# Kernel optimization log

Hardware: AMD Instinct MI355X
Metric: run time of the kernel (lower is better)

## Reference

```python
import jax, jax.numpy as jnp
import numpy as np

Q = 4096  # num_quantizing
E = 256   # quantizing_dim


def setup_inputs() -> dict:
    key = jax.random.key(0)
    kx, kw = jax.random.split(key)
    x = jax.random.normal(kx, (16, 2048, E), dtype=jnp.float32)
    # nn.init.normal_(weight, mean=0.0, std=0.001)
    weight = 0.001 * jax.random.normal(kw, (Q, E), dtype=jnp.float32)
    return {"x": x, "weight": weight}


def reference(x, weight):
    # x: (*, E), weight: (Q, E)
    input_shape = x.shape
    xf = x.reshape(-1, weight.shape[1])  # (N, E)
    # Squared L2 distance via norm expansion (same argmin as sum(delta^2)):
    x2 = jnp.sum(xf * xf, axis=1, keepdims=True)          # (N, 1)
    w2 = jnp.sum(weight * weight, axis=1)                  # (Q,)
    dist = x2 - 2.0 * (xf @ weight.T) + w2                 # (N, Q)
    q_idx = jnp.argmin(dist, axis=1)                       # (N,)
    q_data = weight[q_idx]                                 # (N, E)
    return q_data.reshape(input_shape), q_idx.reshape(input_shape[:-1])
```

## Files before the change

### kernel.cpp

```cpp
#include <hip/hip_runtime.h>
#include <cfloat>
#include <climits>

constexpr int E  = 256;
constexpr int Qn = 4096;
constexpr float WSCALE = 4096.0f;


typedef _Float16 half8  __attribute__((ext_vector_type(8)));
typedef _Float16 half4v __attribute__((ext_vector_type(4)));
typedef float    f32x16 __attribute__((ext_vector_type(16)));

#define GAS __attribute__((address_space(1)))
#define LAS __attribute__((address_space(3)))

#define NEG_INF __int_as_float(0xFF800000)

__device__ inline bool lexlt(float a, int ai, float b, int bi) {
    return a < b || (a == b && ai < bi);
}

__global__ __launch_bounds__(256) void prep_kernel(
    const float* __restrict__ x, const float* __restrict__ w,
    _Float16* __restrict__ A16, _Float16* __restrict__ B16,
    float* __restrict__ w2, int nxblocks)
{
    int blk  = blockIdx.x;
    int sub  = threadIdx.x >> 6;
    int lane = threadIdx.x & 63;
    bool isX = blk < nxblocks;
    int row  = (isX ? blk : blk - nxblocks) * 4 + sub;

    const float* src = isX ? x : w;
    float4 v = *(const float4*)(src + (size_t)row * E + lane * 4);

    if (!isX) {
        float s = v.x * v.x + v.y * v.y + v.z * v.z + v.w * v.w;
        #pragma unroll
        for (int off = 32; off; off >>= 1) s += __shfl_xor(s, off);
        if (lane == 0) w2[row] = s;
    }

    float sc = isX ? 1.0f : WSCALE;
    half4v h = { (_Float16)(v.x * sc), (_Float16)(v.y * sc),
                 (_Float16)(v.z * sc), (_Float16)(v.w * sc) };
    _Float16* dst16 = (isX ? A16 : B16) + (size_t)row * 256;
    *(half4v*)(dst16 + lane * 4) = h;
}

__device__ inline void ins4max(float K[4], float k) {
    #pragma unroll
    for (int t = 0; t < 4; ++t) {
        float mx = fmaxf(K[t], k);
        k = fminf(K[t], k);
        K[t] = mx;
    }
}

union SmemU {
    _Float16 buf[4][2][128][64];
    float2 mergeS[128 * 16];
};

#define KSTEP(T, VMSTR, Q, H)                                              \
  {                                                                        \
    asm volatile("s_waitcnt " VMSTR ::: "memory");                         \
    __builtin_amdgcn_s_barrier();                                          \
    asm volatile("" ::: "memory");                                         \
    const int t_ = (T);                                                    \
    if (t_ + 3 < 64) stage_t(t_ + 3);                                      \
    const _Float16* Wb = &sm.buf[t_ & 3][0][0][0];                         \
    if ((H) == 0) { acc0 = (f32x16){}; acc1 = (f32x16){}; }                \
    __builtin_amdgcn_s_setprio(1);                                         \
    _Pragma("unroll")                                                      \
    for (int ktl = 0; ktl < 2; ++ktl)                                      \
      _Pragma("unroll")                                                    \
      for (int s = 0; s < 4; ++s) {                                        \
        int kc = 2 * s + lh;                                               \
        half8 wf = *(const half8*)(Wb + ktl * 8192                         \
                      + fr * 64 + ((kc ^ frsw) << 3));                     \
        acc0 = __builtin_amdgcn_mfma_f32_32x32x16_f16(                     \
                   wf, xf[0][2 * (H) + ktl][s], acc0, 0, 0, 0);            \
        acc1 = __builtin_amdgcn_mfma_f32_32x32x16_f16(                     \
                   wf, xf[1][2 * (H) + ktl][s], acc1, 0, 0, 0);            \
      }                                                                    \
    __builtin_amdgcn_s_setprio(0);                                         \
    if ((H) == 1) {                                                        \
      const int ct_ = t_ >> 1;                                             \
      _Pragma("unroll")                                                    \
      for (int r = 0; r < 16; ++r) {                                       \
        int crow = (r & 3) + 8 * (r >> 2) + 4 * lh;                        \
        int qg   = ct_ * 128 + cwg * 32 + crow;                            \
        float pk0 = __int_as_float(                                        \
            (__float_as_int(acc0[r]) & 0xFFFFF000) | qg);                  \
        t2[0][(Q)] = __builtin_amdgcn_fmed3f(t1[0][(Q)], t2[0][(Q)], pk0); \
        t1[0][(Q)] = fmaxf(t1[0][(Q)], pk0);                               \
        float pk1 = __int_as_float(                                        \
            (__float_as_int(acc1[r]) & 0xFFFFF000) | qg);                  \
        t2[1][(Q)] = __builtin_amdgcn_fmed3f(t1[1][(Q)], t2[1][(Q)], pk1); \
        t1[1][(Q)] = fmaxf(t1[1][(Q)], pk1);                               \
      }                                                                    \
    }                                                                      \
  }

__global__ __launch_bounds__(512, 2) void vq_mfma_kernel(
    const _Float16* __restrict__ A16,
    const _Float16* __restrict__ B16,
    float4* __restrict__ top4)
{
    __shared__ SmemU sm;

    const int tid  = threadIdx.x;
    const int wv   = tid >> 6;
    const int lane = tid & 63;
    const int l31  = lane & 31;
    const int lh   = lane >> 5;
    const int rb   = blockIdx.x;

    const int cwg = wv & 3;
    const int rg  = wv >> 2;

    const int srow = lane >> 3;
    const int schk = lane & 7;

    const _Float16* Ab16 = A16 + (size_t)rb * 128 * 256;

    auto stage_half = [&](const _Float16* src, int slot, int h) {
        #pragma unroll
        for (int ktl = 0; ktl < 2; ++ktl)
            #pragma unroll
            for (int i = 0; i < 2; ++i) {
                int row  = i * 64 + wv * 8 + srow;
                int gchk = schk ^ (row & 7);
                const _Float16* g = src + (size_t)row * 256
                                    + (2 * h + ktl) * 64 + gchk * 8;
                __builtin_amdgcn_global_load_lds((const GAS void*)g,
                    (LAS void*)(&sm.buf[slot][ktl][i * 64 + wv * 8][0]),
                    16, 0, 0);
            }
    };
    auto stage_t = [&](int t) {
        stage_half(B16 + (size_t)(t >> 1) * 128 * 256, t & 3, t & 1);
    };

    stage_half(Ab16, 0, 0);
    stage_half(Ab16, 1, 1);
    __syncthreads();

    half8 xf[2][4][4];
    #pragma unroll
    for (int n = 0; n < 2; ++n)
        #pragma unroll
        for (int kt = 0; kt < 4; ++kt)
            #pragma unroll
            for (int s = 0; s < 4; ++s) {
                int xr = rg * 64 + n * 32 + l31;
                int kc = 2 * s + lh;
                xf[n][kt][s] = *(const half8*)(&sm.buf[kt >> 1][kt & 1][0][0]
                                + xr * 64 + ((kc ^ (xr & 7)) << 3));
            }
    __syncthreads();

    stage_t(0); stage_t(1); stage_t(2);

    float t1[2][4], t2[2][4];
    #pragma unroll
    for (int n = 0; n < 2; ++n)
        #pragma unroll
        for (int q = 0; q < 4; ++q) { t1[n][q] = NEG_INF; t2[n][q] = NEG_INF; }

    const int fr   = cwg * 32 + l31;
    const int frsw = fr & 7;

    f32x16 acc0, acc1;

    #pragma unroll
    for (int q = 0; q < 4; ++q) {
        const int nct = (q == 3) ? 7 : 8;
        for (int ctt = 0; ctt < nct; ++ctt) {
            const int t0 = (q * 8 + ctt) * 2;
            KSTEP(t0,     "vmcnt(8)", q, 0);
            KSTEP(t0 + 1, "vmcnt(8)", q, 1);
        }
    }
    KSTEP(62, "vmcnt(4)", 3, 0);
    KSTEP(63, "vmcnt(0)", 3, 1);

    #pragma unroll
    for (int n = 0; n < 2; ++n)
        #pragma unroll
        for (int q = 0; q < 4; ++q) {
            float o1 = __shfl_xor(t1[n][q], 32);
            float o2 = __shfl_xor(t2[n][q], 32);
            float m1 = fmaxf(t1[n][q], o1);
            float m2 = __builtin_amdgcn_fmed3f(t1[n][q], o1,
                                               fmaxf(t2[n][q], o2));
            t1[n][q] = m1; t2[n][q] = m2;
        }

    __syncthreads();

    if (lh == 0) {
        #pragma unroll
        for (int n = 0; n < 2; ++n) {
            int row = rg * 64 + n * 32 + l31;
            #pragma unroll
            for (int q = 0; q < 4; ++q)
                sm.mergeS[row * 16 + cwg * 4 + q] =
                    make_float2(t1[n][q], t2[n][q]);
        }
    }
    __syncthreads();

    if (tid < 128) {
        float K[4] = { NEG_INF, NEG_INF, NEG_INF, NEG_INF };
        #pragma unroll
        for (int sl = 0; sl < 16; ++sl) {
            float2 a = sm.mergeS[tid * 16 + sl];
            ins4max(K, a.x);
            ins4max(K, a.y);
        }
        top4[(size_t)rb * 128 + tid] = make_float4(K[0], K[1], K[2], K[3]);
    }
}

__global__ __launch_bounds__(256) void finalize_kernel(
    const float4* __restrict__ top4, const float* __restrict__ x,
    const float* __restrict__ w, const float* __restrict__ w2,
    float* __restrict__ qdata, float* __restrict__ qidx)
{
    int row  = blockIdx.x * 4 + (threadIdx.x >> 6);
    int lane = threadIdx.x & 63;

    float4 c4 = top4[row];
    int chosen[4] = { __float_as_int(c4.x) & 0xFFF,
                      __float_as_int(c4.y) & 0xFFF,
                      __float_as_int(c4.z) & 0xFFF,
                      __float_as_int(c4.w) & 0xFFF };

    float4 xv = *(const float4*)(x + (size_t)row * E + lane * 4);
    float s2 = xv.x * xv.x + xv.y * xv.y + xv.z * xv.z + xv.w * xv.w;
    float d[4];
    #pragma unroll
    for (int j = 0; j < 4; ++j) {
        float4 wv = *(const float4*)(w + (size_t)chosen[j] * E + lane * 4);
        d[j] = xv.x * wv.x + xv.y * wv.y + xv.z * wv.z + xv.w * wv.w;
    }
    #pragma unroll
    for (int off = 32; off; off >>= 1) {
        s2 += __shfl_xor(s2, off);
        #pragma unroll
        for (int j = 0; j < 4; ++j) d[j] += __shfl_xor(d[j], off);
    }

    float bs = FLT_MAX; int win = INT_MAX;
    #pragma unroll
    for (int j = 0; j < 4; ++j) {
        float s = (s2 - 2.0f * d[j]) + w2[chosen[j]];
        if (lexlt(s, chosen[j], bs, win)) { bs = s; win = chosen[j]; }
    }

    if (lane == 0) qidx[row] = (float)win;
    *(float4*)(qdata + (size_t)row * E + lane * 4) =
        *(const float4*)(w + (size_t)win * E + lane * 4);
}

constexpr int FBM = 64, FBN = 128, FBK = 64, FPAD = 4, FTH = 256;

__global__ __launch_bounds__(64) void row_sumsq_kernel(const float* __restrict__ src,
                                                       float* __restrict__ dst) {
    int row = blockIdx.x, lane = threadIdx.x;
    float4 v = ((const float4*)(src + (size_t)row * E))[lane];
    float s = v.x * v.x + v.y * v.y + v.z * v.z + v.w * v.w;
    #pragma unroll
    for (int off = 32; off > 0; off >>= 1) s += __shfl_down(s, off);
    if (lane == 0) dst[row] = s;
}

__global__ __launch_bounds__(FTH) void vq_fallback_kernel(
    const float* __restrict__ x, const float* __restrict__ w,
    const float* __restrict__ x2, const float* __restrict__ w2,
    float* __restrict__ qdata, float* __restrict__ qidx)
{
    __shared__ float xs[FBM][FBK + FPAD];
    __shared__ float ws[FBN][FBK + FPAD];
    __shared__ float redS[FBM][16];
    __shared__ int   redC[FBM][16];
    __shared__ int   bestC[FBM];

    const int tid = threadIdx.x, tr = tid >> 4, tc = tid & 15;
    const int r0 = blockIdx.x * FBM;
    float best[4]; int bidx[4];
    #pragma unroll
    for (int i = 0; i < 4; ++i) { best[i] = FLT_MAX; bidx[i] = 0x7FFFFFFF; }
    float x2r[4];
    #pragma unroll
    for (int i = 0; i < 4; ++i) x2r[i] = x2[r0 + tr + 16 * i];

    for (int qt = 0; qt < Qn / FBN; ++qt) {
        const int c0 = qt * FBN;
        float acc[4][8];
        #pragma unroll
        for (int i = 0; i < 4; ++i)
            #pragma unroll
            for (int j = 0; j < 8; ++j) acc[i][j] = 0.f;
        for (int kt = 0; kt < E / FBK; ++kt) {
            __syncthreads();
            const int kk = (tid & 15) * 4, rr = tid >> 4;
            #pragma unroll
            for (int m = 0; m < 4; ++m)
                *(float4*)&xs[m * 16 + rr][kk] =
                    *(const float4*)(x + (size_t)(r0 + m * 16 + rr) * E + kt * FBK + kk);
            #pragma unroll
            for (int m = 0; m < 8; ++m)
                *(float4*)&ws[m * 16 + rr][kk] =
                    *(const float4*)(w + (size_t)(c0 + m * 16 + rr) * E + kt * FBK + kk);
            __syncthreads();
            #pragma unroll
            for (int k4 = 0; k4 < FBK / 4; ++k4) {
                float4 a[4], bb[8];
                #pragma unroll
                for (int i = 0; i < 4; ++i) a[i] = *(const float4*)&xs[tr + 16 * i][k4 * 4];
                #pragma unroll
                for (int j = 0; j < 8; ++j) bb[j] = *(const float4*)&ws[tc + 16 * j][k4 * 4];
                #pragma unroll
                for (int i = 0; i < 4; ++i)
                    #pragma unroll
                    for (int j = 0; j < 8; ++j) {
                        acc[i][j] += a[i].x * bb[j].x; acc[i][j] += a[i].y * bb[j].y;
                        acc[i][j] += a[i].z * bb[j].z; acc[i][j] += a[i].w * bb[j].w;
                    }
            }
        }
        #pragma unroll
        for (int i = 0; i < 4; ++i)
            #pragma unroll
            for (int j = 0; j < 8; ++j) {
                int c = c0 + tc + 16 * j;
                float s = (x2r[i] - 2.0f * acc[i][j]) + w2[c];
                if (s < best[i]) { best[i] = s; bidx[i] = c; }
            }
    }
    #pragma unroll
    for (int i = 0; i < 4; ++i) { redS[tr + 16 * i][tc] = best[i]; redC[tr + 16 * i][tc] = bidx[i]; }
    __syncthreads();
    if (tid < FBM) {
        float bs = FLT_MAX; int bc = 0x7FFFFFFF;
        #pragma unroll
        for (int t = 0; t < 16; ++t) {
            float s = redS[tid][t]; int c = redC[tid][t];
            if (s < bs || (s == bs && c < bc)) { bs = s; bc = c; }
        }
        qidx[r0 + tid] = (float)bc; bestC[tid] = bc;
    }
    __syncthreads();
    for (int it = 0; it < FBM / 4; ++it) {
        int row = it * 4 + (tid >> 6), c = bestC[row], kk = (tid & 63) * 4;
        *(float4*)(qdata + (size_t)(r0 + row) * E + kk) = *(const float4*)(w + (size_t)c * E + kk);
    }
}

extern "C" void kernel_launch(void* const* d_in, const int* in_sizes, int n_in,
                              void* d_out, int out_size, void* d_ws, size_t ws_size,
                              hipStream_t stream) {
    const float* x = (const float*)d_in[0];
    const float* w = (const float*)d_in[1];
    const int N = in_sizes[0] / E;

    float* qdata = (float*)d_out;
    float* qidx  = (float*)d_out + (size_t)N * E;

    size_t off = 0;
    auto carve = [&](size_t bytes) { size_t p = off; off += (bytes + 255) & ~(size_t)255; return p; };
    size_t oA16 = carve((size_t)N  * 256 * sizeof(_Float16));
    size_t oB16 = carve((size_t)Qn * 256 * sizeof(_Float16));
    size_t ow2  = carve((size_t)Qn * sizeof(float));
    size_t oT   = carve((size_t)N * sizeof(float4));
    size_t ox2f = carve((size_t)N * sizeof(float));

    if (ws_size >= off && (N % 128) == 0) {
        char* ws = (char*)d_ws;
        _Float16* A16 = (_Float16*)(ws + oA16);
        _Float16* B16 = (_Float16*)(ws + oB16);
        float* w2    = (float*)(ws + ow2);
        float4* top4 = (float4*)(ws + oT);

        prep_kernel<<<N / 4 + Qn / 4, 256, 0, stream>>>(x, w, A16, B16, w2, N / 4);
        vq_mfma_kernel<<<N / 128, 512, 0, stream>>>(A16, B16, top4);
        finalize_kernel<<<N / 4, 256, 0, stream>>>(top4, x, w, w2, qdata, qidx);
    } else {
        float* x2 = (float*)d_ws;
        float* w2 = x2 + N;
        row_sumsq_kernel<<<N, 64, 0, stream>>>(x, x2);
        row_sumsq_kernel<<<Qn, 64, 0, stream>>>(w, w2);
        vq_fallback_kernel<<<N / FBM, FTH, 0, stream>>>(x, w, x2, w2, qdata, qidx);
    }
}
```

Before: 176.6 us.

## Split codebook across two blocks per row tile and merge top-4 in finalize

Each row tile of 128 now launches two blocks, each scanning half of the codebook (2048 entries), and the two partial top-4 lists are merged in the finalize kernel. The shared-memory weight ring shrinks from four slots to two, and occupancy hint rises to four blocks per CU. The manual vmcnt-tracked triple-buffered prefetch is replaced by a single-ahead prefetch with a full __syncthreads per step. This aims to improve CU fill and occupancy, but it reloads the x tile twice, adds more barrier stalls with less prefetch depth, and doubles the top4 traffic.

```diff
diff --git a/kernel.cpp b/kernel.cpp
--- a/kernel.cpp
+++ b/kernel.cpp
@@ -58,18 +58,15 @@
 }
 
 union SmemU {
-    _Float16 buf[4][2][128][64];
+    _Float16 buf[2][2][128][64];
     float2 mergeS[128 * 16];
 };
 
-#define KSTEP(T, VMSTR, Q, H)                                              \
+#define KSTEP(T, Q, H)                                                     \
   {                                                                        \
-    asm volatile("s_waitcnt " VMSTR ::: "memory");                         \
-    __builtin_amdgcn_s_barrier();                                          \
-    asm volatile("" ::: "memory");                                         \
     const int t_ = (T);                                                    \
-    if (t_ + 3 < 64) stage_t(t_ + 3);                                      \
-    const _Float16* Wb = &sm.buf[t_ & 3][0][0][0];                         \
+    if (t_ + 1 < 32) stage_t(t_ + 1);                                      \
+    const _Float16* Wb = &sm.buf[t_ & 1][0][0][0];                         \
     if ((H) == 0) { acc0 = (f32x16){}; acc1 = (f32x16){}; }                \
     __builtin_amdgcn_s_setprio(1);                                         \
     _Pragma("unroll")                                                      \
@@ -90,7 +87,7 @@
       _Pragma("unroll")                                                    \
       for (int r = 0; r < 16; ++r) {                                       \
         int crow = (r & 3) + 8 * (r >> 2) + 4 * lh;                        \
-        int qg   = ct_ * 128 + cwg * 32 + crow;                            \
+        int qg   = cwbase + ct_ * 128 + cwg * 32 + crow;                   \
         float pk0 = __int_as_float(                                        \
             (__float_as_int(acc0[r]) & 0xFFFFF000) | qg);                  \
         t2[0][(Q)] = __builtin_amdgcn_fmed3f(t1[0][(Q)], t2[0][(Q)], pk0); \
@@ -101,9 +98,10 @@
         t1[1][(Q)] = fmaxf(t1[1][(Q)], pk1);                               \
       }                                                                    \
     }                                                                      \
+    __syncthreads();                                                       \
   }
 
-__global__ __launch_bounds__(512, 2) void vq_mfma_kernel(
+__global__ __launch_bounds__(512, 4) void vq_mfma_kernel(
     const _Float16* __restrict__ A16,
     const _Float16* __restrict__ B16,
     float4* __restrict__ top4)
@@ -115,15 +113,18 @@
     const int lane = tid & 63;
     const int l31  = lane & 31;
     const int lh   = lane >> 5;
-    const int rb   = blockIdx.x;
+    const int ch   = blockIdx.x;
+    const int rb   = blockIdx.y;
 
     const int cwg = wv & 3;
     const int rg  = wv >> 2;
+    const int cwbase = ch * 2048;
 
     const int srow = lane >> 3;
     const int schk = lane & 7;
 
     const _Float16* Ab16 = A16 + (size_t)rb * 128 * 256;
+    const _Float16* B16h = B16 + (size_t)ch * 2048 * 256;
 
     auto stage_half = [&](const _Float16* src, int slot, int h) {
         #pragma unroll
@@ -140,7 +141,7 @@
             }
     };
     auto stage_t = [&](int t) {
-        stage_half(B16 + (size_t)(t >> 1) * 128 * 256, t & 3, t & 1);
+        stage_half(B16h + (size_t)(t >> 1) * 128 * 256, t & 1, t & 1);
     };
 
     stage_half(Ab16, 0, 0);
@@ -161,8 +162,6 @@
             }
     __syncthreads();
 
-    stage_t(0); stage_t(1); stage_t(2);
-
     float t1[2][4], t2[2][4];
     #pragma unroll
     for (int n = 0; n < 2; ++n)
@@ -174,17 +173,17 @@
 
     f32x16 acc0, acc1;
 
-    #pragma unroll
-    for (int q = 0; q < 4; ++q) {
-        const int nct = (q == 3) ? 7 : 8;
-        for (int ctt = 0; ctt < nct; ++ctt) {
-            const int t0 = (q * 8 + ctt) * 2;
-            KSTEP(t0,     "vmcnt(8)", q, 0);
-            KSTEP(t0 + 1, "vmcnt(8)", q, 1);
-        }
-    }
-    KSTEP(62, "vmcnt(4)", 3, 0);
-    KSTEP(63, "vmcnt(0)", 3, 1);
+    stage_t(0);
+    __syncthreads();
+
+    #pragma unroll
+    for (int q = 0; q < 4; ++q)
+        #pragma unroll
+        for (int ctt = 0; ctt < 4; ++ctt) {
+            const int t0 = (q * 4 + ctt) * 2;
+            KSTEP(t0,     q, 0);
+            KSTEP(t0 + 1, q, 1);
+        }
 
     #pragma unroll
     for (int n = 0; n < 2; ++n)
@@ -198,8 +197,6 @@
             t1[n][q] = m1; t2[n][q] = m2;
         }
 
-    __syncthreads();
-
     if (lh == 0) {
         #pragma unroll
         for (int n = 0; n < 2; ++n) {
@@ -220,7 +217,8 @@
             ins4max(K, a.x);
             ins4max(K, a.y);
         }
-        top4[(size_t)rb * 128 + tid] = make_float4(K[0], K[1], K[2], K[3]);
+        top4[((size_t)rb * 128 + tid) * 2 + ch] =
+            make_float4(K[0], K[1], K[2], K[3]);
     }
 }
 
@@ -232,11 +230,16 @@
     int row  = blockIdx.x * 4 + (threadIdx.x >> 6);
     int lane = threadIdx.x & 63;
 
-    float4 c4 = top4[row];
-    int chosen[4] = { __float_as_int(c4.x) & 0xFFF,
-                      __float_as_int(c4.y) & 0xFFF,
-                      __float_as_int(c4.z) & 0xFFF,
-                      __float_as_int(c4.w) & 0xFFF };
+    float4 a = top4[(size_t)row * 2 + 0];
+    float4 b = top4[(size_t)row * 2 + 1];
+    float K[4] = { NEG_INF, NEG_INF, NEG_INF, NEG_INF };
+    ins4max(K, a.x); ins4max(K, a.y); ins4max(K, a.z); ins4max(K, a.w);
+    ins4max(K, b.x); ins4max(K, b.y); ins4max(K, b.z); ins4max(K, b.w);
+
+    int chosen[4] = { __float_as_int(K[0]) & 0xFFF,
+                      __float_as_int(K[1]) & 0xFFF,
+                      __float_as_int(K[2]) & 0xFFF,
+                      __float_as_int(K[3]) & 0xFFF };
 
     float4 xv = *(const float4*)(x + (size_t)row * E + lane * 4);
     float s2 = xv.x * xv.x + xv.y * xv.y + xv.z * xv.z + xv.w * xv.w;
@@ -375,7 +378,7 @@
     size_t oA16 = carve((size_t)N  * 256 * sizeof(_Float16));
     size_t oB16 = carve((size_t)Qn * 256 * sizeof(_Float16));
     size_t ow2  = carve((size_t)Qn * sizeof(float));
-    size_t oT   = carve((size_t)N * sizeof(float4));
+    size_t oT   = carve((size_t)N * 2 * sizeof(float4));
     size_t ox2f = carve((size_t)N * sizeof(float));
 
     if (ws_size >= off && (N % 128) == 0) {
@@ -386,7 +389,7 @@
         float4* top4 = (float4*)(ws + oT);
 
         prep_kernel<<<N / 4 + Qn / 4, 256, 0, stream>>>(x, w, A16, B16, w2, N / 4);
-        vq_mfma_kernel<<<N / 128, 512, 0, stream>>>(A16, B16, top4);
+        vq_mfma_kernel<<<dim3(2, N / 128), 512, 0, stream>>>(A16, B16, top4);
         finalize_kernel<<<N / 4, 256, 0, stream>>>(top4, x, w, w2, qdata, qidx);
     } else {
         float* x2 = (float*)d_ws;
```

New measurement: 347.3 us. 96.7% more time.
